# Kernel optimization log

Hardware: AMD Instinct MI355X
Metric: run time of the kernel (lower is better)

The kernel has to match this reference:

```python
import jax, jax.numpy as jnp
import numpy as np

EPS = 1e-5
NEG = -1e9

def rmsnorm(x, g, eps=EPS):
    x32 = x.astype(jnp.float32)
    n = x32 * jax.lax.rsqrt(jnp.mean(x32 * x32, axis=-1, keepdims=True) + eps)
    return g * n.astype(x.dtype)

def setup_inputs() -> dict:
    key = jax.random.key(0)
    ks = jax.random.split(key, 10)
    B, S, D, H = 2, 2048, 768, 12
    F = 4 * D
    s = 0.02
    return {
        "x": jax.random.normal(ks[0], (B, S, D), jnp.float32),
        "mask": jax.random.randint(ks[1], (B, S, S), 0, 2, jnp.int32),
        "wq": jax.random.normal(ks[2], (D, D), jnp.float32) * s,
        "wk": jax.random.normal(ks[3], (D, D), jnp.float32) * s,
        "wv": jax.random.normal(ks[4], (D, D), jnp.float32) * s,
        "wo": jax.random.normal(ks[5], (D, D), jnp.float32) * s,
        "w1": jax.random.normal(ks[6], (F, D), jnp.float32) * s,
        "w2": jax.random.normal(ks[7], (D, F), jnp.float32) * s,
        "w3": jax.random.normal(ks[8], (F, D), jnp.float32) * s,
        "g_attn": jnp.ones((D,), jnp.float32),
        "g_ffn": jnp.ones((D,), jnp.float32),
    }

def reference(x, mask, wq, wk, wv, wo, w1, w2, w3, g_attn, g_ffn):
    B, S, D = x.shape
    H = 12
    Dk = D // H
    # --- attention sub-block (pre-norm) ---
    xn = rmsnorm(x, g_attn)
    # torch Linear: y = x @ W^T; split heads -> [B,H,S,Dk]
    q = (xn @ wq.T).reshape(B, S, H, Dk).transpose(0, 2, 1, 3)
    k = (xn @ wk.T).reshape(B, S, H, Dk).transpose(0, 2, 1, 3)
    v = (xn @ wv.T).reshape(B, S, H, Dk).transpose(0, 2, 1, 3)
    scores = jnp.einsum("bhqd,bhkd->bhqk", q, k) / jnp.sqrt(jnp.float32(Dk))
    scores = jnp.where(mask[:, None, :, :] == 0, jnp.float32(NEG), scores)
    probs = jax.nn.softmax(scores, axis=-1)  # dropout p=0.0 -> identity
    attn = jnp.einsum("bhqk,bhkd->bhqd", probs, v)
    attn = attn.transpose(0, 2, 1, 3).reshape(B, S, D)
    h = x + attn @ wo.T
    # --- SwiGLU FFN sub-block (pre-norm) ---
    hn = rmsnorm(h, g_ffn)
    ffn = (jax.nn.silu(hn @ w1.T) * (hn @ w3.T)) @ w2.T
    return h + ffn
```

## Files before the change

### kernel.cpp

```cpp
#include <hip/hip_runtime.h>
#include <hip/hip_bf16.h>

#define S_LEN 2048
#define D_MODEL 768
#define NH 12
#define DK 64
#define F_DIM 3072
#define BATCH 2
#define M_ROWS (BATCH * S_LEN)

typedef __bf16 bf16x8 __attribute__((ext_vector_type(8)));
typedef float floatx4 __attribute__((ext_vector_type(4)));
typedef unsigned short u16;
typedef unsigned long long u64;

__device__ inline float bf2f(u16 u) {
    union { unsigned int i; float f; } x; x.i = ((unsigned int)u) << 16; return x.f;
}
__device__ inline u16 f2bf(float f) {
    union { float f; unsigned int i; } x; x.f = f;
    unsigned int r = x.i + 0x7fffu + ((x.i >> 16) & 1u);
    return (u16)(r >> 16);
}
__device__ __forceinline__ bf16x8 as_bf16x8(uint4 v) {
    union { uint4 u; bf16x8 b; } c; c.u = v; return c.b;
}

__device__ __forceinline__ void ldsload16(const u16* g, u16* l) {
    __builtin_amdgcn_global_load_lds(
        (const __attribute__((address_space(1))) unsigned int*)g,
        (__attribute__((address_space(3))) unsigned int*)l, 16, 0, 0);
}

__global__ __launch_bounds__(256)
void cvt_all(const float4* __restrict__ wq, const float4* __restrict__ wk,
             const float4* __restrict__ wv, const float4* __restrict__ wo,
             const float4* __restrict__ w1, const float4* __restrict__ w2,
             const float4* __restrict__ w3,
             ushort4* wqb, ushort4* wkb, ushort4* wvb, ushort4* wob,
             ushort4* w13f, ushort4* w2b) {
    const int WS4 = (D_MODEL * D_MODEL) / 4;
    const int WB4 = (F_DIM * D_MODEL) / 4;
    const int RW4 = D_MODEL / 4;
    int i = blockIdx.x * 256 + threadIdx.x;
    const float4* src; ushort4* dst; int off, doff;
    if (i < 4 * WS4) {
        int s = i / WS4; off = i - s * WS4; doff = off;
        src = (s == 0) ? wq : (s == 1) ? wk : (s == 2) ? wv : wo;
        dst = (s == 0) ? wqb : (s == 1) ? wkb : (s == 2) ? wvb : wob;
    } else {
        int j = i - 4 * WS4; int s = j / WB4; off = j - s * WB4;
        if (s == 1) { src = w2; dst = w2b; doff = off; }
        else {
            src = (s == 0) ? w1 : w3;
            dst = w13f;
            int which = (s == 0) ? 0 : 1;
            int row = off / RW4, c4 = off - row * RW4;
            int k = c4 * 4;
            int n_tile = row >> 4, nl = row & 15;
            int k_tile = k >> 5, quad = (k >> 3) & 3, jj = k & 7;
            int lane = quad * 16 + nl;
            int f = (n_tile * 24 + k_tile) * 2 + which;
            doff = (f * 512 + lane * 8 + jj) >> 2;
        }
    }
    float4 v = src[off];
    ushort4 o;
    o.x = f2bf(v.x); o.y = f2bf(v.y); o.z = f2bf(v.z); o.w = f2bf(v.w);
    dst[doff] = o;
}

__global__ __launch_bounds__(256)
void mask_bits(const int* __restrict__ m, u64* __restrict__ bits) {
    size_t gid = (size_t)blockIdx.x * 256 + threadIdx.x;
    u64 b = __ballot(m[gid] != 0);
    if ((threadIdx.x & 63) == 0) bits[gid >> 6] = b;
}

__global__ __launch_bounds__(256)
void rmsnorm_k(const float* __restrict__ x, const float* __restrict__ g, u16* __restrict__ out) {
    int row = blockIdx.x;
    const float* xr = x + (size_t)row * D_MODEL;
    u16* orow = out + (size_t)row * D_MODEL;
    int t = threadIdx.x;
    float v0 = xr[t];
    float v1 = xr[t + 256];
    float v2 = xr[t + 512];
    float ss = v0 * v0 + v1 * v1 + v2 * v2;
    #pragma unroll
    for (int off = 1; off < 64; off <<= 1) ss += __shfl_xor(ss, off);
    __shared__ float red[4];
    if ((t & 63) == 0) red[t >> 6] = ss;
    __syncthreads();
    float tot = red[0] + red[1] + red[2] + red[3];
    float scale = rsqrtf(tot * (1.0f / (float)D_MODEL) + 1e-5f);
    orow[t]       = f2bf(g[t]       * v0 * scale);
    orow[t + 256] = f2bf(g[t + 256] * v1 * scale);
    orow[t + 512] = f2bf(g[t + 512] * v2 * scale);
}

__global__ __launch_bounds__(256, 3)
void gemm_f1(const u16* __restrict__ A, const u16* __restrict__ W13f,
             u16* __restrict__ Cout) {
    const int K = D_MODEL, N = F_DIM;
    __shared__ u16 As[2][64][32];

    int t = threadIdx.x;
    int w = t >> 6, lane = t & 63;
    int lrow = lane & 15, quad = lane >> 4;

    int lid = blockIdx.y * 24 + blockIdx.x;
    int xcd = lid & 7, s = lid >> 3;
    int nb = xcd * 3 + (s % 3);
    int mb = s / 3;
    int mBase = mb * 64;
    int ntile0 = nb * 8 + w * 2;

    int srow = lane >> 2, scol = (lane & 3) * 8;
    const u16* Ag = A + (size_t)(mBase + w * 16 + srow) * K + scol;
    const uint4* Bf = (const uint4*)W13f;

    auto stageA = [&](int k0, int b) {
        ldsload16(Ag + k0, &As[b][w * 16][0]);
    };

    floatx4 zero = {0.f, 0.f, 0.f, 0.f};
    floatx4 acc[4][2], acc2[4][2];
    #pragma unroll
    for (int r = 0; r < 4; ++r)
        #pragma unroll
        for (int c = 0; c < 2; ++c) { acc[r][c] = zero; acc2[r][c] = zero; }

    stageA(0, 0);
    int cur = 0;
    for (int kt = 0; kt < 24; ++kt) {
        uint4 b1v[2], b3v[2];
        #pragma unroll
        for (int c = 0; c < 2; ++c) {
            int f = ((ntile0 + c) * 24 + kt) * 2;
            b1v[c] = Bf[(size_t)f * 64 + lane];
            b3v[c] = Bf[(size_t)(f + 1) * 64 + lane];
        }
        __syncthreads();
        if (kt + 1 < 24) stageA((kt + 1) * 32, cur ^ 1);

        bf16x8 af[4];
        #pragma unroll
        for (int r = 0; r < 4; ++r) af[r] = *(const bf16x8*)&As[cur][r * 16 + lrow][quad * 8];
        #pragma unroll
        for (int c = 0; c < 2; ++c) {
            bf16x8 b1f = as_bf16x8(b1v[c]);
            bf16x8 b3f = as_bf16x8(b3v[c]);
            #pragma unroll
            for (int r = 0; r < 4; ++r) {
                acc[r][c]  = __builtin_amdgcn_mfma_f32_16x16x32_bf16(af[r], b1f, acc[r][c], 0, 0, 0);
                acc2[r][c] = __builtin_amdgcn_mfma_f32_16x16x32_bf16(af[r], b3f, acc2[r][c], 0, 0, 0);
            }
        }
        cur ^= 1;
    }

    #pragma unroll
    for (int r = 0; r < 4; ++r) {
        #pragma unroll
        for (int c = 0; c < 2; ++c) {
            #pragma unroll
            for (int j = 0; j < 4; ++j) {
                int grow = mBase + r * 16 + quad * 4 + j;
                int gcol = nb * 128 + w * 32 + c * 16 + lrow;
                float a = acc[r][c][j];
                Cout[(size_t)grow * N + gcol] = f2bf((a / (1.0f + __expf(-a))) * acc2[r][c][j]);
            }
        }
    }
}

__global__ __launch_bounds__(256, 3)
void gemm64(const u16* __restrict__ A, const u16* __restrict__ B1,
            const float* __restrict__ R, float* __restrict__ Cout, int N, int K) {
    __shared__ u16 As[2][64][32];
    __shared__ u16 Bs[2][64][32];

    int t = threadIdx.x;
    int w = t >> 6, lane = t & 63;
    int mBase = blockIdx.y * 64, nBase = blockIdx.x * 64;
    int lrow = lane & 15, quad = lane >> 4;
    int wm = (w >> 1) * 32, wn = (w & 1) * 32;

    int srow = lane >> 2, scol = (lane & 3) * 8;
    const u16* Ag = A  + (size_t)(mBase + w * 16 + srow) * K + scol;
    const u16* Bg = B1 + (size_t)(nBase + w * 16 + srow) * K + scol;

    auto stage = [&](int k0, int b) {
        ldsload16(Ag + k0, &As[b][w * 16][0]);
        ldsload16(Bg + k0, &Bs[b][w * 16][0]);
    };

    floatx4 zero = {0.f, 0.f, 0.f, 0.f};
    floatx4 acc[2][2];
    #pragma unroll
    for (int r = 0; r < 2; ++r)
        #pragma unroll
        for (int c = 0; c < 2; ++c) acc[r][c] = zero;

    stage(0, 0);
    int cur = 0;
    for (int k0 = 0; k0 < K; k0 += 32) {
        __syncthreads();
        if (k0 + 32 < K) stage(k0 + 32, cur ^ 1);

        bf16x8 af[2], bf[2];
        #pragma unroll
        for (int r = 0; r < 2; ++r) af[r] = *(const bf16x8*)&As[cur][wm + r * 16 + lrow][quad * 8];
        #pragma unroll
        for (int c = 0; c < 2; ++c) bf[c] = *(const bf16x8*)&Bs[cur][wn + c * 16 + lrow][quad * 8];
        #pragma unroll
        for (int r = 0; r < 2; ++r)
            #pragma unroll
            for (int c = 0; c < 2; ++c)
                acc[r][c] = __builtin_amdgcn_mfma_f32_16x16x32_bf16(af[r], bf[c], acc[r][c], 0, 0, 0);
        cur ^= 1;
    }

    #pragma unroll
    for (int r = 0; r < 2; ++r) {
        #pragma unroll
        for (int c = 0; c < 2; ++c) {
            #pragma unroll
            for (int j = 0; j < 4; ++j) {
                int grow = mBase + wm + r * 16 + quad * 4 + j;
                int gcol = nBase + wn + c * 16 + lrow;
                size_t idx = (size_t)grow * N + gcol;
                Cout[idx] = acc[r][c][j] + R[idx];
            }
        }
    }
}

__global__ __launch_bounds__(256, 4)
void gemm_qkv(const u16* __restrict__ A, const u16* __restrict__ wq,
              const u16* __restrict__ wk, const u16* __restrict__ wv,
              u16* __restrict__ qb, u16* __restrict__ kb, u16* __restrict__ vt) {
    const int K = D_MODEL;
    __shared__ u16 As[2][64][32];
    __shared__ u16 Bs[2][128][32];

    int t = threadIdx.x;
    int w = t >> 6, lane = t & 63;
    int nb = blockIdx.x;
    int which = nb / 6;
    int mBase = blockIdx.y * 64, nBase = (nb % 6) * 128;
    const u16* B1 = (which == 0) ? wq : (which == 1) ? wk : wv;
    int lrow = lane & 15, quad = lane >> 4;
    int wm = (w >> 1) * 32, wn = (w & 1) * 64;

    int srow = lane >> 2, scol = (lane & 3) * 8;
    const u16* Ag = A  + (size_t)(mBase + w * 16 + srow) * K + scol;
    const u16* Bg = B1 + (size_t)(nBase + w * 32 + srow) * K + scol;

    auto stage = [&](int k0, int b) {
        ldsload16(Ag + k0, &As[b][w * 16][0]);
        ldsload16(Bg + k0, &Bs[b][w * 32][0]);
        ldsload16(Bg + (size_t)16 * K + k0, &Bs[b][w * 32 + 16][0]);
    };

    floatx4 zero = {0.f, 0.f, 0.f, 0.f};
    floatx4 acc[2][4];
    #pragma unroll
    for (int r = 0; r < 2; ++r)
        #pragma unroll
        for (int c = 0; c < 4; ++c) acc[r][c] = zero;

    stage(0, 0);
    int cur = 0;
    for (int k0 = 0; k0 < K; k0 += 32) {
        __syncthreads();
        if (k0 + 32 < K) stage(k0 + 32, cur ^ 1);
        bf16x8 af[2];
        #pragma unroll
        for (int r = 0; r < 2; ++r) af[r] = *(const bf16x8*)&As[cur][wm + r * 16 + lrow][quad * 8];
        #pragma unroll
        for (int c = 0; c < 4; ++c) {
            bf16x8 bfr = *(const bf16x8*)&Bs[cur][wn + c * 16 + lrow][quad * 8];
            #pragma unroll
            for (int r = 0; r < 2; ++r)
                acc[r][c] = __builtin_amdgcn_mfma_f32_16x16x32_bf16(af[r], bfr, acc[r][c], 0, 0, 0);
        }
        cur ^= 1;
    }

    u16* dst = (which == 0) ? qb : kb;
    const float qscale = 0.18033688011112042f;
    #pragma unroll
    for (int r = 0; r < 2; ++r) {
        #pragma unroll
        for (int c = 0; c < 4; ++c) {
            #pragma unroll
            for (int j = 0; j < 4; ++j) {
                int grow = mBase + wm + r * 16 + quad * 4 + j;
                int gcol = nBase + wn + c * 16 + lrow;
                float val = acc[r][c][j];
                if (which == 2) {
                    int bb = grow >> 11, s = grow & 2047;
                    int hh = gcol >> 6, d = gcol & 63;
                    vt[((((size_t)bb * NH + hh) * DK + d) << 11) + s] = f2bf(val);
                } else {
                    if (which == 0) val *= qscale;
                    dst[(size_t)grow * D_MODEL + gcol] = f2bf(val);
                }
            }
        }
    }
}

__global__ __launch_bounds__(256)
void attn_mfma(const u16* __restrict__ q, const u16* __restrict__ k,
               const u16* __restrict__ vt, const u64* __restrict__ mbits,
               u16* __restrict__ out) {
    __shared__ u16 Qs0[64][32], Qs1[64][32];
    __shared__ u16 Ks0[64][32], Ks1[64][32];
    __shared__ u16 Vs0[64][32], Vs1[64][32];
    __shared__ u16 PT[4][16][72];

    int t = threadIdx.x;
    int lane = t & 63;
    int w = t >> 6;
    int lrow = lane & 15;
    int quad = lane >> 4;

    int st0 = blockIdx.x * 64;
    int bh = blockIdx.y;
    int h = bh % NH;
    int b = bh / NH;

    const u16* qbase = q + ((size_t)b * S_LEN + st0) * D_MODEL + h * DK;
    const u16* kbase = k + (size_t)b * S_LEN * D_MODEL + h * DK;
    const u16* vbase = vt + (size_t)bh * DK * S_LEN;
    const u64* bw = mbits + ((size_t)b * S_LEN + st0 + w * 16 + lrow) * (S_LEN / 64);

    int srow = lane >> 2;
    int scol = (lane & 3) * 8;

    const u16* qg = qbase + (size_t)(w * 16 + srow) * D_MODEL + scol;
    ldsload16(qg, &Qs0[w * 16][0]);
    ldsload16(qg + 32, &Qs1[w * 16][0]);
    __syncthreads();
    bf16x8 bq0 = *(const bf16x8*)&Qs0[w * 16 + lrow][quad * 8];
    bf16x8 bq1 = *(const bf16x8*)&Qs1[w * 16 + lrow][quad * 8];

    const u16* kg = kbase + (size_t)(w * 16 + srow) * D_MODEL + scol;
    const u16* vg = vbase + (size_t)(w * 16 + srow) * S_LEN + scol;

    bf16x8 ones;
    {
        union { u16 u; __bf16 b; } o; o.u = 0x3F80;
        #pragma unroll
        for (int j = 0; j < 8; ++j) ones[j] = o.b;
    }

    floatx4 zero = {0.f, 0.f, 0.f, 0.f};
    floatx4 Ot[4] = {zero, zero, zero, zero};
    floatx4 Osum = zero;

    for (int kt = 0; kt < S_LEN; kt += 64) {
        u64 mw = bw[kt >> 6];
        unsigned mlo = (unsigned)mw, mhi = (unsigned)(mw >> 32);
        __syncthreads();
        ldsload16(kg + (size_t)kt * D_MODEL, &Ks0[w * 16][0]);
        ldsload16(kg + (size_t)kt * D_MODEL + 32, &Ks1[w * 16][0]);
        ldsload16(vg + kt, &Vs0[w * 16][0]);
        ldsload16(vg + kt + 32, &Vs1[w * 16][0]);
        __syncthreads();

        floatx4 st[4];
        #pragma unroll
        for (int nt = 0; nt < 4; ++nt) {
            bf16x8 ak0 = *(const bf16x8*)&Ks0[nt * 16 + lrow][quad * 8];
            bf16x8 ak1 = *(const bf16x8*)&Ks1[nt * 16 + lrow][quad * 8];
            st[nt] = __builtin_amdgcn_mfma_f32_16x16x32_bf16(ak0, bq0, zero, 0, 0, 0);
            st[nt] = __builtin_amdgcn_mfma_f32_16x16x32_bf16(ak1, bq1, st[nt], 0, 0, 0);
        }

        #pragma unroll
        for (int nt = 0; nt < 4; ++nt) {
            unsigned half = (nt & 2) ? mhi : mlo;
            unsigned tmp = half >> ((nt & 1) * 16 + quad * 4);
            unsigned eu[4];
            #pragma unroll
            for (int j = 0; j < 4; ++j) {
                float e = __builtin_amdgcn_exp2f(st[nt][j]);
                unsigned msk = (unsigned)((int)(tmp << (31 - j)) >> 31);
                eu[j] = __float_as_uint(e) & msk;
            }
            uint2 p;
            p.x = (eu[0] >> 16) | (eu[1] & 0xffff0000u);
            p.y = (eu[2] >> 16) | (eu[3] & 0xffff0000u);
            *(uint2*)&PT[w][lrow][nt * 16 + quad * 4] = p;
        }

        bf16x8 ap0 = *(const bf16x8*)&PT[w][lrow][quad * 8];
        bf16x8 ap1 = *(const bf16x8*)&PT[w][lrow][32 + quad * 8];
        Osum = __builtin_amdgcn_mfma_f32_16x16x32_bf16(ap0, ones, Osum, 0, 0, 0);
        Osum = __builtin_amdgcn_mfma_f32_16x16x32_bf16(ap1, ones, Osum, 0, 0, 0);
        #pragma unroll
        for (int dt = 0; dt < 4; ++dt) {
            bf16x8 bv0 = *(const bf16x8*)&Vs0[dt * 16 + lrow][quad * 8];
            bf16x8 bv1 = *(const bf16x8*)&Vs1[dt * 16 + lrow][quad * 8];
            Ot[dt] = __builtin_amdgcn_mfma_f32_16x16x32_bf16(ap0, bv0, Ot[dt], 0, 0, 0);
            Ot[dt] = __builtin_amdgcn_mfma_f32_16x16x32_bf16(ap1, bv1, Ot[dt], 0, 0, 0);
        }
    }

    float invj[4];
    #pragma unroll
    for (int j = 0; j < 4; ++j) invj[j] = 1.0f / Osum[j];

    u16* obase = out + ((size_t)b * S_LEN + st0 + w * 16) * D_MODEL + h * DK;
    #pragma unroll
    for (int dt = 0; dt < 4; ++dt)
        #pragma unroll
        for (int j = 0; j < 4; ++j)
            obase[(size_t)(quad * 4 + j) * D_MODEL + dt * 16 + lrow] = f2bf(Ot[dt][j] * invj[j]);
}

extern "C" void kernel_launch(void* const* d_in, const int* in_sizes, int n_in,
                              void* d_out, int out_size, void* d_ws, size_t ws_size,
                              hipStream_t stream) {
    const float* x      = (const float*)d_in[0];
    const int*   mask   = (const int*)d_in[1];
    const float* wq     = (const float*)d_in[2];
    const float* wk     = (const float*)d_in[3];
    const float* wv     = (const float*)d_in[4];
    const float* wo     = (const float*)d_in[5];
    const float* w1     = (const float*)d_in[6];
    const float* w2     = (const float*)d_in[7];
    const float* w3     = (const float*)d_in[8];
    const float* g_attn = (const float*)d_in[9];
    const float* g_ffn  = (const float*)d_in[10];
    float* out = (float*)d_out;

    const size_t WSMALL = (size_t)D_MODEL * D_MODEL;
    const size_t WBIG   = (size_t)F_DIM * D_MODEL;
    const size_t MD     = (size_t)M_ROWS * D_MODEL;

    char* ws = (char*)d_ws;
    u16* wqb  = (u16*)ws;            ws += WSMALL * 2;
    u16* wkb  = (u16*)ws;            ws += WSMALL * 2;
    u16* wvb  = (u16*)ws;            ws += WSMALL * 2;
    u16* wob  = (u16*)ws;            ws += WSMALL * 2;
    u16* w13f = (u16*)ws;            ws += WBIG * 2 * 2;
    u16* w2b  = (u16*)ws;            ws += WBIG * 2;
    u16* xn  = (u16*)ws;             ws += MD * 2;
    u16* qb  = (u16*)ws;             ws += MD * 2;
    u16* kb  = (u16*)ws;             ws += MD * 2;
    u16* vb  = (u16*)ws;             ws += MD * 2;
    u16* ao  = (u16*)ws;             ws += MD * 2;
    float* hb = (float*)ws;          ws += MD * 4;
    u64* mb  = (u64*)ws;             ws += (size_t)BATCH * S_LEN * (S_LEN / 64) * 8;
    u16* hn = xn;
    u16* ub = qb;
    (void)ws_size; (void)n_in; (void)in_sizes; (void)out_size;

    dim3 blk(256);

    cvt_all<<<9216, blk, 0, stream>>>((const float4*)wq, (const float4*)wk, (const float4*)wv,
                                      (const float4*)wo, (const float4*)w1, (const float4*)w2,
                                      (const float4*)w3,
                                      (ushort4*)wqb, (ushort4*)wkb, (ushort4*)wvb, (ushort4*)wob,
                                      (ushort4*)w13f, (ushort4*)w2b);
    mask_bits<<<(BATCH * S_LEN * S_LEN) / 256, blk, 0, stream>>>(mask, mb);

    rmsnorm_k<<<M_ROWS, blk, 0, stream>>>(x, g_attn, xn);
    gemm_qkv<<<dim3(18, M_ROWS / 64), blk, 0, stream>>>(xn, wqb, wkb, wvb, qb, kb, vb);
    attn_mfma<<<dim3(S_LEN / 64, BATCH * NH), blk, 0, stream>>>(qb, kb, vb, mb, ao);
    gemm64<<<dim3(D_MODEL / 64, M_ROWS / 64), blk, 0, stream>>>(ao, wob, x, hb, D_MODEL, D_MODEL);
    rmsnorm_k<<<M_ROWS, blk, 0, stream>>>((const float*)hb, g_ffn, hn);
    gemm_f1<<<dim3(24, M_ROWS / 64), blk, 0, stream>>>(hn, w13f, ub);
    gemm64<<<dim3(D_MODEL / 64, M_ROWS / 64), blk, 0, stream>>>(ub, w2b, hb, out, D_MODEL, F_DIM);
}
```

Baseline: 352.1 us.

## Double-buffer K/V tiles in attention to overlap loads with MFMA compute

The K and V shared-memory tiles in the attention kernel become double-buffered. The next tile, and its mask word, are now prefetched at the start of each iteration while the current tile is computed. Each iteration now needs one barrier instead of two, and global-load latency can hide behind the QK, softmax and PV MFMA work. The cost is twice the LDS used for K/V, which may lower occupancy.

```diff
diff --git a/kernel.cpp b/kernel.cpp
--- a/kernel.cpp
+++ b/kernel.cpp
@@ -318,8 +318,8 @@
                const u16* __restrict__ vt, const u64* __restrict__ mbits,
                u16* __restrict__ out) {
     __shared__ u16 Qs0[64][32], Qs1[64][32];
-    __shared__ u16 Ks0[64][32], Ks1[64][32];
-    __shared__ u16 Vs0[64][32], Vs1[64][32];
+    __shared__ u16 Ks0[2][64][32], Ks1[2][64][32];
+    __shared__ u16 Vs0[2][64][32], Vs1[2][64][32];
     __shared__ u16 PT[4][16][72];
 
     int t = threadIdx.x;
@@ -341,16 +341,24 @@
     int srow = lane >> 2;
     int scol = (lane & 3) * 8;
 
+    const u16* kg = kbase + (size_t)(w * 16 + srow) * D_MODEL + scol;
+    const u16* vg = vbase + (size_t)(w * 16 + srow) * S_LEN + scol;
+
+    auto stageKV = [&](int kt, int bsel) {
+        ldsload16(kg + (size_t)kt * D_MODEL, &Ks0[bsel][w * 16][0]);
+        ldsload16(kg + (size_t)kt * D_MODEL + 32, &Ks1[bsel][w * 16][0]);
+        ldsload16(vg + kt, &Vs0[bsel][w * 16][0]);
+        ldsload16(vg + kt + 32, &Vs1[bsel][w * 16][0]);
+    };
+
     const u16* qg = qbase + (size_t)(w * 16 + srow) * D_MODEL + scol;
     ldsload16(qg, &Qs0[w * 16][0]);
     ldsload16(qg + 32, &Qs1[w * 16][0]);
+    stageKV(0, 0);
     __syncthreads();
     bf16x8 bq0 = *(const bf16x8*)&Qs0[w * 16 + lrow][quad * 8];
     bf16x8 bq1 = *(const bf16x8*)&Qs1[w * 16 + lrow][quad * 8];
 
-    const u16* kg = kbase + (size_t)(w * 16 + srow) * D_MODEL + scol;
-    const u16* vg = vbase + (size_t)(w * 16 + srow) * S_LEN + scol;
-
     bf16x8 ones;
     {
         union { u16 u; __bf16 b; } o; o.u = 0x3F80;
@@ -362,21 +370,18 @@
     floatx4 Ot[4] = {zero, zero, zero, zero};
     floatx4 Osum = zero;
 
+    u64 mw = bw[0];
+    int cur = 0;
     for (int kt = 0; kt < S_LEN; kt += 64) {
-        u64 mw = bw[kt >> 6];
+        if (kt + 64 < S_LEN) stageKV(kt + 64, cur ^ 1);
+        u64 mw_next = (kt + 64 < S_LEN) ? bw[(kt >> 6) + 1] : 0ull;
         unsigned mlo = (unsigned)mw, mhi = (unsigned)(mw >> 32);
-        __syncthreads();
-        ldsload16(kg + (size_t)kt * D_MODEL, &Ks0[w * 16][0]);
-        ldsload16(kg + (size_t)kt * D_MODEL + 32, &Ks1[w * 16][0]);
-        ldsload16(vg + kt, &Vs0[w * 16][0]);
-        ldsload16(vg + kt + 32, &Vs1[w * 16][0]);
-        __syncthreads();
 
         floatx4 st[4];
         #pragma unroll
         for (int nt = 0; nt < 4; ++nt) {
-            bf16x8 ak0 = *(const bf16x8*)&Ks0[nt * 16 + lrow][quad * 8];
-            bf16x8 ak1 = *(const bf16x8*)&Ks1[nt * 16 + lrow][quad * 8];
+            bf16x8 ak0 = *(const bf16x8*)&Ks0[cur][nt * 16 + lrow][quad * 8];
+            bf16x8 ak1 = *(const bf16x8*)&Ks1[cur][nt * 16 + lrow][quad * 8];
             st[nt] = __builtin_amdgcn_mfma_f32_16x16x32_bf16(ak0, bq0, zero, 0, 0, 0);
             st[nt] = __builtin_amdgcn_mfma_f32_16x16x32_bf16(ak1, bq1, st[nt], 0, 0, 0);
         }
@@ -404,11 +409,15 @@
         Osum = __builtin_amdgcn_mfma_f32_16x16x32_bf16(ap1, ones, Osum, 0, 0, 0);
         #pragma unroll
         for (int dt = 0; dt < 4; ++dt) {
-            bf16x8 bv0 = *(const bf16x8*)&Vs0[dt * 16 + lrow][quad * 8];
-            bf16x8 bv1 = *(const bf16x8*)&Vs1[dt * 16 + lrow][quad * 8];
+            bf16x8 bv0 = *(const bf16x8*)&Vs0[cur][dt * 16 + lrow][quad * 8];
+            bf16x8 bv1 = *(const bf16x8*)&Vs1[cur][dt * 16 + lrow][quad * 8];
             Ot[dt] = __builtin_amdgcn_mfma_f32_16x16x32_bf16(ap0, bv0, Ot[dt], 0, 0, 0);
             Ot[dt] = __builtin_amdgcn_mfma_f32_16x16x32_bf16(ap1, bv1, Ot[dt], 0, 0, 0);
         }
+
+        __syncthreads();
+        cur ^= 1;
+        mw = mw_next;
     }
 
     float invj[4];
```

Result: no change. 352.2 us (+0.1%).
